# Kernel tuning notes

Hardware: AMD Instinct MI355X
Metric: run time of the kernel (lower is better)

The kernel has to match this reference:

```python
import jax, jax.numpy as jnp
import numpy as np

D_MODEL = 256
NUM_ITEMS = 16
TOPK = 4
TAU = 0.1
EPS = 1e-12  # torch F.normalize eps


def _l2norm(x):
    n = jnp.sqrt(jnp.sum(x * x, axis=-1, keepdims=True))
    return x / jnp.maximum(n, EPS)


def setup_inputs() -> dict:
    key = jax.random.key(0)
    kq, km = jax.random.split(key)
    queries = jax.random.normal(kq, (32, 4096, D_MODEL), dtype=jnp.float32)
    memory = jax.random.normal(km, (NUM_ITEMS, D_MODEL), dtype=jnp.float32)
    memory = _l2norm(memory)  # init normalizes the bank to unit vectors
    return {"queries": queries, "memory": memory}


def reference(queries, memory):
    # queries: [B, Np, d]; memory: [M, d]
    q = _l2norm(queries)
    m = _l2norm(memory)
    sim = jnp.einsum('bnd,md->bnm', q, m) / TAU            # [B, Np, M]
    topk_sim, topk_idx = jax.lax.top_k(sim, TOPK)          # [B, Np, k]
    topk_w = jax.nn.softmax(topk_sim, axis=-1)             # [B, Np, k]
    mem_sel = memory[topk_idx]                             # [B, Np, k, d] (raw memory, matching torch)
    retrieved = jnp.einsum('bnk,bnkd->bnd', topk_w, mem_sel)
    sim_max = jnp.max(sim, axis=-1, keepdims=True)         # [B, Np, 1]
    return retrieved, sim_max
```

## Files before the change

### kernel.cpp

```cpp
#include <hip/hip_runtime.h>
#include <math.h>

#define D 256
#define M 16
#define TAU 0.1f
#define EPSN 1e-12f
#define MEM_STRIDE 260
#define WAVES_PER_BLOCK 4
#define ROWS_PER_BLOCK 64
#define ITERS (ROWS_PER_BLOCK / WAVES_PER_BLOCK)

__global__ __launch_bounds__(256, 4)
void epm_kernel(const float* __restrict__ q, const float* __restrict__ mem,
                float* __restrict__ ret_out, float* __restrict__ smax_out)
{
    __shared__ __align__(16) float mem_lds[M * MEM_STRIDE];
    __shared__ float inv_nm_lds[M];
    __shared__ __align__(16) float qbuf[WAVES_PER_BLOCK * 4 * 68];

    const int tid  = threadIdx.x;
    const int wave = tid >> 6;
    const int lane = tid & 63;
    const int mIdx = lane & 15;
    const int cIdx = lane >> 4;

    {
        const float4* m4 = (const float4*)mem;
        #pragma unroll
        for (int p = 0; p < 4; ++p) {
            int vi  = p * 256 + tid;
            int row = vi >> 6;
            int col = (vi & 63) * 4;
            float4 v = m4[vi];
            *(float4*)&mem_lds[row * MEM_STRIDE + col] = v;
        }
    }
    __syncthreads();

    if (tid < M) {
        const float4* r4 = (const float4*)&mem_lds[tid * MEM_STRIDE];
        float ss = 0.f;
        #pragma unroll
        for (int j = 0; j < D / 4; ++j) {
            float4 v = r4[j];
            ss += v.x * v.x + v.y * v.y + v.z * v.z + v.w * v.w;
        }
        inv_nm_lds[tid] = 1.0f / fmaxf(sqrtf(ss), EPSN);
    }
    __syncthreads();

    float4 memr[16];
    {
        const float4* src = (const float4*)&mem_lds[mIdx * MEM_STRIDE + cIdx * 64];
        #pragma unroll
        for (int j = 0; j < 16; ++j) memr[j] = src[j];
    }
    const float scale_m = inv_nm_lds[mIdx] * (1.0f / TAU);

    float* myq = &qbuf[wave * (4 * 68)];
    const int row0 = blockIdx.x * ROWS_PER_BLOCK;

    int r = row0 + wave;
    float4 qv = ((const float4*)q)[(size_t)r * 64 + lane];

    for (int t = 0; t < ITERS; ++t) {
        int tn = (t + 1 < ITERS) ? (t + 1) : t;
        int rown = row0 + tn * 4 + wave;
        float4 qnext = ((const float4*)q)[(size_t)rown * 64 + lane];

        float ss = qv.x * qv.x + qv.y * qv.y + qv.z * qv.z + qv.w * qv.w;
        #pragma unroll
        for (int d = 32; d >= 1; d >>= 1) ss += __shfl_xor(ss, d);
        float inv_nq = 1.0f / fmaxf(sqrtf(ss), EPSN);

        *(float4*)&myq[(lane >> 4) * 68 + (lane & 15) * 4] = qv;
        __syncthreads();

        float acc = 0.f;
        {
            const float4* qs = (const float4*)&myq[cIdx * 68];
            #pragma unroll
            for (int j = 0; j < 16; ++j) {
                float4 a = qs[j];
                float4 b = memr[j];
                acc += a.x * b.x + a.y * b.y + a.z * b.z + a.w * b.w;
            }
        }
        acc += __shfl_xor(acc, 16);
        acc += __shfl_xor(acc, 32);
        float sim = acc * inv_nq * scale_m;

        float smax = sim;
        #pragma unroll
        for (int d = 8; d >= 1; d >>= 1) smax = fmaxf(smax, __shfl_xor(smax, d));

        int cnt = 0;
        #pragma unroll
        for (int d = 1; d < 16; ++d) {
            float ov = __shfl_xor(sim, d);
            int om = mIdx ^ d;
            cnt += (ov > sim || (ov == sim && om < mIdx)) ? 1 : 0;
        }

        float tw[4];
        int   tm[4];
        #pragma unroll
        for (int k = 0; k < 4; ++k) {
            unsigned long long ball = __ballot(cnt == k);
            int src = (int)__builtin_ctzll(ball);
            float sv = __shfl(sim, src);
            tm[k] = src & 15;
            tw[k] = __expf(sv - smax);
        }
        float invd = 1.0f / (tw[0] + tw[1] + tw[2] + tw[3]);

        float4 accv = make_float4(0.f, 0.f, 0.f, 0.f);
        #pragma unroll
        for (int k = 0; k < 4; ++k) {
            float4 mv = *(const float4*)&mem_lds[tm[k] * MEM_STRIDE + 4 * lane];
            float w = tw[k];
            accv.x += w * mv.x; accv.y += w * mv.y;
            accv.z += w * mv.z; accv.w += w * mv.w;
        }
        accv.x *= invd; accv.y *= invd; accv.z *= invd; accv.w *= invd;

        ((float4*)ret_out)[(size_t)r * 64 + lane] = accv;
        if (lane == 0) smax_out[r] = smax;

        qv = qnext;
        r = row0 + (t + 1) * 4 + wave;
        __syncthreads();
    }
}

extern "C" void kernel_launch(void* const* d_in, const int* in_sizes, int n_in,
                              void* d_out, int out_size, void* d_ws, size_t ws_size,
                              hipStream_t stream) {
    const float* queries = (const float*)d_in[0];
    const float* memory  = (const float*)d_in[1];
    float* out = (float*)d_out;

    const int rows = in_sizes[0] / D;
    float* ret_out  = out;
    float* smax_out = out + (size_t)rows * D;

    const int blocks = rows / ROWS_PER_BLOCK;
    epm_kernel<<<blocks, 64 * WAVES_PER_BLOCK, 0, stream>>>(queries, memory, ret_out, smax_out);
}
```

Before: 250.9 us.

## Batch rows per wave, do top-k per lane, drop block-wide barriers

Each wave now handles 16 contiguous rows. For each row it computes the similarities, using a DPP-based wave reduction for the query norm, and stores them to LDS. Afterwards one lane per row runs a sorted-insertion top-4, packing the index into the low mantissa bits to break ties, and writes the softmax weights and indices to LDS. A separate loop then gathers memory rows and writes the outputs. This removes the per-row __syncthreads and the shuffle-heavy rank, ballot and shuffle selection. In exchange it adds LDS traffic, a serial 16-step selection on only 16 lanes, and a slight perturbation of the sim values used for top-k and smax from the bit packing.

New measurement: 242.4 us. -3.4%, faster.

```diff
diff --git a/kernel.cpp b/kernel.cpp
--- a/kernel.cpp
+++ b/kernel.cpp
@@ -6,9 +6,26 @@
 #define TAU 0.1f
 #define EPSN 1e-12f
 #define MEM_STRIDE 260
-#define WAVES_PER_BLOCK 4
-#define ROWS_PER_BLOCK 64
-#define ITERS (ROWS_PER_BLOCK / WAVES_PER_BLOCK)
+#define NWAVES 4
+#define BATCH 16
+#define ROWS_PER_BLOCK (NWAVES * BATCH)
+
+template <int CTRL, int ROW_MASK, int BANK_MASK>
+__device__ __forceinline__ float dpp_add(float x) {
+    int xi = __builtin_bit_cast(int, x);
+    int mi = __builtin_amdgcn_update_dpp(0, xi, CTRL, ROW_MASK, BANK_MASK, true);
+    return x + __builtin_bit_cast(float, mi);
+}
+__device__ __forceinline__ float wave_sum(float x) {
+    x = dpp_add<0x111, 0xf, 0xf>(x);
+    x = dpp_add<0x112, 0xf, 0xf>(x);
+    x = dpp_add<0x114, 0xf, 0xe>(x);
+    x = dpp_add<0x118, 0xf, 0xc>(x);
+    x = dpp_add<0x142, 0xa, 0xf>(x);
+    x = dpp_add<0x143, 0xc, 0xf>(x);
+    int t = __builtin_amdgcn_readlane(__builtin_bit_cast(int, x), 63);
+    return __builtin_bit_cast(float, t);
+}
 
 __global__ __launch_bounds__(256, 4)
 void epm_kernel(const float* __restrict__ q, const float* __restrict__ mem,
@@ -16,13 +33,17 @@
 {
     __shared__ __align__(16) float mem_lds[M * MEM_STRIDE];
     __shared__ float inv_nm_lds[M];
-    __shared__ __align__(16) float qbuf[WAVES_PER_BLOCK * 4 * 68];
+    __shared__ __align__(16) float qbuf[NWAVES][4 * 68];
+    __shared__ float simbuf[NWAVES][M * 17];
+    __shared__ float nbuf[NWAVES][BATCH];
+    __shared__ __align__(16) float wbuf[NWAVES][BATCH * 4];
+    __shared__ int   mbuf[NWAVES][BATCH];
 
     const int tid  = threadIdx.x;
-    const int wave = tid >> 6;
+    const int wv   = tid >> 6;
     const int lane = tid & 63;
-    const int mIdx = lane & 15;
-    const int cIdx = lane >> 4;
+    const int m    = lane & 15;
+    const int c    = lane >> 4;
 
     {
         const float4* m4 = (const float4*)mem;
@@ -51,85 +72,92 @@
 
     float4 memr[16];
     {
-        const float4* src = (const float4*)&mem_lds[mIdx * MEM_STRIDE + cIdx * 64];
+        const float4* src = (const float4*)&mem_lds[m * MEM_STRIDE + c * 64];
         #pragma unroll
         for (int j = 0; j < 16; ++j) memr[j] = src[j];
     }
-    const float scale_m = inv_nm_lds[mIdx] * (1.0f / TAU);
+    const float scale_m = inv_nm_lds[m] * (1.0f / TAU);
 
-    float* myq = &qbuf[wave * (4 * 68)];
-    const int row0 = blockIdx.x * ROWS_PER_BLOCK;
+    const int wave_row0 = blockIdx.x * ROWS_PER_BLOCK + wv * BATCH;
+    float* myq = &qbuf[wv][0];
+    float* simw = &simbuf[wv][0];
 
-    int r = row0 + wave;
-    float4 qv = ((const float4*)q)[(size_t)r * 64 + lane];
+    float4 qv = ((const float4*)q)[(size_t)wave_row0 * 64 + lane];
+    #pragma unroll
+    for (int r = 0; r < BATCH; ++r) {
+        float4 qn = qv;
+        if (r + 1 < BATCH)
+            qn = ((const float4*)q)[(size_t)(wave_row0 + r + 1) * 64 + lane];
 
-    for (int t = 0; t < ITERS; ++t) {
-        int tn = (t + 1 < ITERS) ? (t + 1) : t;
-        int rown = row0 + tn * 4 + wave;
-        float4 qnext = ((const float4*)q)[(size_t)rown * 64 + lane];
-
-        float ss = qv.x * qv.x + qv.y * qv.y + qv.z * qv.z + qv.w * qv.w;
-        #pragma unroll
-        for (int d = 32; d >= 1; d >>= 1) ss += __shfl_xor(ss, d);
-        float inv_nq = 1.0f / fmaxf(sqrtf(ss), EPSN);
+        float sq = qv.x * qv.x + qv.y * qv.y + qv.z * qv.z + qv.w * qv.w;
+        float ss = wave_sum(sq);
+        if (lane == 0) nbuf[wv][r] = ss;
 
         *(float4*)&myq[(lane >> 4) * 68 + (lane & 15) * 4] = qv;
-        __syncthreads();
 
         float acc = 0.f;
-        {
-            const float4* qs = (const float4*)&myq[cIdx * 68];
-            #pragma unroll
-            for (int j = 0; j < 16; ++j) {
-                float4 a = qs[j];
-                float4 b = memr[j];
-                acc += a.x * b.x + a.y * b.y + a.z * b.z + a.w * b.w;
-            }
+        const float4* qs = (const float4*)&myq[c * 68];
+        #pragma unroll
+        for (int j = 0; j < 16; ++j) {
+            float4 a = qs[j];
+            float4 b = memr[j];
+            acc += a.x * b.x + a.y * b.y + a.z * b.z + a.w * b.w;
         }
         acc += __shfl_xor(acc, 16);
         acc += __shfl_xor(acc, 32);
-        float sim = acc * inv_nq * scale_m;
+        if (c == 0) simw[m * 17 + r] = acc * scale_m;
+        qv = qn;
+    }
 
-        float smax = sim;
+    if (lane < BATCH) {
+        const int r = lane;
+        float ssq = nbuf[wv][r];
+        float inv_nq = 1.0f / fmaxf(sqrtf(ssq), EPSN);
+
+        float k0 = -INFINITY, k1 = -INFINITY, k2 = -INFINITY, k3 = -INFINITY;
         #pragma unroll
-        for (int d = 8; d >= 1; d >>= 1) smax = fmaxf(smax, __shfl_xor(smax, d));
+        for (int mm = 0; mm < M; ++mm) {
+            float s = simw[mm * 17 + r] * inv_nq;
+            int si = (__builtin_bit_cast(int, s) & ~15) | (15 - mm);
+            float ks = __builtin_bit_cast(float, si);
+            bool g0 = ks > k0, g1 = ks > k1, g2 = ks > k2, g3 = ks > k3;
+            float n3 = g2 ? k2 : (g3 ? ks : k3);
+            float n2 = g1 ? k1 : (g2 ? ks : k2);
+            float n1 = g0 ? k0 : (g1 ? ks : k1);
+            float n0 = g0 ? ks : k0;
+            k0 = n0; k1 = n1; k2 = n2; k3 = n3;
+        }
+        int m0 = 15 - (__builtin_bit_cast(int, k0) & 15);
+        int m1 = 15 - (__builtin_bit_cast(int, k1) & 15);
+        int m2 = 15 - (__builtin_bit_cast(int, k2) & 15);
+        int m3 = 15 - (__builtin_bit_cast(int, k3) & 15);
 
-        int cnt = 0;
-        #pragma unroll
-        for (int d = 1; d < 16; ++d) {
-            float ov = __shfl_xor(sim, d);
-            int om = mIdx ^ d;
-            cnt += (ov > sim || (ov == sim && om < mIdx)) ? 1 : 0;
-        }
+        float w0 = 1.0f;
+        float w1 = __expf(k1 - k0);
+        float w2 = __expf(k2 - k0);
+        float w3 = __expf(k3 - k0);
+        float invd = 1.0f / (w0 + w1 + w2 + w3);
 
-        float tw[4];
-        int   tm[4];
-        #pragma unroll
-        for (int k = 0; k < 4; ++k) {
-            unsigned long long ball = __ballot(cnt == k);
-            int src = (int)__builtin_ctzll(ball);
-            float sv = __shfl(sim, src);
-            tm[k] = src & 15;
-            tw[k] = __expf(sv - smax);
-        }
-        float invd = 1.0f / (tw[0] + tw[1] + tw[2] + tw[3]);
+        *(float4*)&wbuf[wv][r * 4] = make_float4(w0 * invd, w1 * invd, w2 * invd, w3 * invd);
+        mbuf[wv][r] = m0 | (m1 << 8) | (m2 << 16) | (m3 << 24);
 
+        smax_out[wave_row0 + r] = k0;
+    }
+
+    #pragma unroll
+    for (int r = 0; r < BATCH; ++r) {
+        float4 w = *(const float4*)&wbuf[wv][r * 4];
+        int mp = mbuf[wv][r];
         float4 accv = make_float4(0.f, 0.f, 0.f, 0.f);
         #pragma unroll
         for (int k = 0; k < 4; ++k) {
-            float4 mv = *(const float4*)&mem_lds[tm[k] * MEM_STRIDE + 4 * lane];
-            float w = tw[k];
-            accv.x += w * mv.x; accv.y += w * mv.y;
-            accv.z += w * mv.z; accv.w += w * mv.w;
+            int mk = (mp >> (8 * k)) & 15;
+            float wk = (k == 0) ? w.x : (k == 1) ? w.y : (k == 2) ? w.z : w.w;
+            float4 mv = *(const float4*)&mem_lds[mk * MEM_STRIDE + 4 * lane];
+            accv.x += wk * mv.x; accv.y += wk * mv.y;
+            accv.z += wk * mv.z; accv.w += wk * mv.w;
         }
-        accv.x *= invd; accv.y *= invd; accv.z *= invd; accv.w *= invd;
-
-        ((float4*)ret_out)[(size_t)r * 64 + lane] = accv;
-        if (lane == 0) smax_out[r] = smax;
-
-        qv = qnext;
-        r = row0 + (t + 1) * 4 + wave;
-        __syncthreads();
+        ((float4*)ret_out)[(size_t)(wave_row0 + r) * 64 + lane] = accv;
     }
 }
 
@@ -145,5 +173,5 @@
     float* smax_out = out + (size_t)rows * D;
 
     const int blocks = rows / ROWS_PER_BLOCK;
-    epm_kernel<<<blocks, 64 * WAVES_PER_BLOCK, 0, stream>>>(queries, memory, ret_out, smax_out);
+    epm_kernel<<<blocks, 64 * NWAVES, 0, stream>>>(queries, memory, ret_out, smax_out);
 }
```
